# Optimization experiments

Hardware: AMD Instinct MI355X
Metric: run time of the kernel (lower is better)

Reference implementation:

```python
import jax, jax.numpy as jnp
import numpy as np

B, C, S, L = 8, 512, 2048, 8921


def setup_inputs() -> dict:
    key = jax.random.key(0)
    k1, k2, k3, k4, k5 = jax.random.split(key, 5)
    return {
        "encoded": jax.random.normal(k1, (B, C, S), dtype=jnp.float32),
        "W_attn": jax.random.normal(k2, (L, C), dtype=jnp.float32) * 0.02,
        "b_attn": jax.random.normal(k3, (L,), dtype=jnp.float32) * 0.02,
        "W_cls": jax.random.normal(k4, (L, C), dtype=jnp.float32) * 0.02,
        "b_cls": jax.random.normal(k5, (L,), dtype=jnp.float32) * 0.02,
    }


def reference(encoded, W_attn, b_attn, W_cls, b_cls):
    # encoded: (B, C, S). Linear over channels after transpose -> scores (B, S, L)
    scores = jnp.einsum("bcs,lc->bsl", encoded, W_attn) + b_attn
    # softmax over the sequence dimension (dim=1 of (B, S, L))
    weights = jax.nn.softmax(scores, axis=1)
    # context: (B, L, S) @ (B, S, C) -> (B, L, C)
    context = jnp.einsum("bsl,bcs->blc", weights, encoded)
    # per-label diagonal classifier: elementwise multiply with (L, C) weight, reduce C
    logits = jnp.sum(context * W_cls, axis=2) + b_cls  # (B, L)
    return logits
```

## Files before the change

### kernel.cpp

```cpp
#include <hip/hip_runtime.h>
#include <hip/hip_bf16.h>
#include <stdint.h>

#define B_ 8
#define C_ 512
#define S_ 2048
#define L_ 8921
#define LTILE 128
#define NLT 70
#define BS 128
#define SCHUNK 512
#define NSC 4
#define BK 64
#define ROUNDS 32

using f32x4 = __attribute__((ext_vector_type(4))) float;
using s16x8 = __attribute__((ext_vector_type(8))) short;

static __device__ __forceinline__ unsigned short f2bf(float f) {
    union { float f; uint32_t u; } a; a.f = f;
    uint32_t u = a.u;
    return (unsigned short)((u + 0x7fffu + ((u >> 16) & 1u)) >> 16);
}

__global__ void cvt_w(const float* __restrict__ src, unsigned short* __restrict__ dst, int n4) {
    int i = blockIdx.x * 256 + threadIdx.x;
    if (i >= n4) return;
    float4 v = ((const float4*)src)[i];
    ushort4 o;
    o.x = f2bf(v.x); o.y = f2bf(v.y); o.z = f2bf(v.z); o.w = f2bf(v.w);
    ((ushort4*)dst)[i] = o;
}

__global__ void cvt_e(const float* __restrict__ enc, unsigned short* __restrict__ ebt) {
    __shared__ float tile[64][65];
    int x = blockIdx.x;
    int ct = (x & 7) * 64;
    int st = ((x >> 3) & 31) * 64;
    int b  = x >> 8;
    int t = threadIdx.x;
    const float* src = enc + (size_t)b * C_ * S_;
    #pragma unroll
    for (int it = 0; it < 16; ++it) {
        int idx = it * 256 + t;
        int rc = idx >> 6, rs = idx & 63;
        tile[rc][rs] = src[(size_t)(ct + rc) * S_ + st + rs];
    }
    __syncthreads();
    unsigned short* dst = ebt + (size_t)b * S_ * C_;
    #pragma unroll
    for (int it = 0; it < 16; ++it) {
        int idx = it * 256 + t;
        int rs = idx >> 6, rc = idx & 63;
        dst[(size_t)(st + rs) * C_ + ct + rc] = f2bf(tile[rc][rs]);
    }
}

__global__ __launch_bounds__(256, 2) void attn_main(
    const unsigned short* __restrict__ ebt,
    const unsigned short* __restrict__ wa,
    const unsigned short* __restrict__ wc,
    float* __restrict__ pnum, float* __restrict__ pden)
{
    __shared__ __align__(16) unsigned char sE[32768];

    const int tid  = threadIdx.x;
    const int lane = tid & 63;
    const int wave = tid >> 6;

    const int x  = blockIdx.x;
    const int lt = x >> 5;
    const int rb = x & 31;
    const int b  = rb >> 2;
    const int sc = rb & 3;
    const int l0 = lt * LTILE;

    int rowOff[2];
    #pragma unroll
    for (int mf = 0; mf < 2; ++mf) {
        int gl = l0 + wave * 32 + mf * 16 + (lane & 15);
        if (gl > L_ - 1) gl = L_ - 1;
        rowOff[mf] = gl * C_ + ((lane >> 4) << 3);
    }

    const size_t ebase = (size_t)b * S_ * C_;
    const int kgsrcE = (((lane & 7) ^ ((lane >> 3) & 7)) << 3);
    const int rowPart = (lane & 15) << 7;
    const int laneQ = lane >> 4;
    const int laneX = lane & 7;

    struct W4 { s16x8 a0, a1, c0, c1; };
    auto loadW = [&](int rr, int k) -> W4 {
        const int co = ((rr & 7) << 6) + (k << 5);
        W4 w;
        w.a0 = *(const s16x8*)(wa + rowOff[0] + co);
        w.a1 = *(const s16x8*)(wa + rowOff[1] + co);
        w.c0 = *(const s16x8*)(wc + rowOff[0] + co);
        w.c1 = *(const s16x8*)(wc + rowOff[1] + co);
        return w;
    };

    auto stageE = [&](int rr2) {
        const int c0s = (rr2 & 7) << 6;
        const int sBase = sc * SCHUNK + (rr2 >> 3) * BS;
        unsigned char* dbase = sE + ((rr2 & 1) << 14);
        #pragma unroll
        for (int jj = 0; jj < 4; ++jj) {
            const int j = wave * 4 + jj;
            const int sg = sBase + j * 8 + (lane >> 3);
            const unsigned short* g = ebt + ebase + (size_t)sg * C_ + c0s + kgsrcE;
            __builtin_amdgcn_global_load_lds(
                (__attribute__((address_space(1))) void*)g,
                (__attribute__((address_space(3))) void*)(dbase + j * 1024),
                16, 0, 0);
        }
    };

    f32x4 accS[2][8], accV[2][8];
    #pragma unroll
    for (int mf = 0; mf < 2; ++mf)
        #pragma unroll
        for (int nf = 0; nf < 8; ++nf) {
            accS[mf][nf] = (f32x4){0.f, 0.f, 0.f, 0.f};
            accV[mf][nf] = (f32x4){0.f, 0.f, 0.f, 0.f};
        }
    float numAcc[2][4], denAcc[2][4];
    #pragma unroll
    for (int mf = 0; mf < 2; ++mf)
        #pragma unroll
        for (int r = 0; r < 4; ++r) { numAcc[mf][r] = 0.f; denAcc[mf][r] = 0.f; }

    stageE(0);
    W4 wcur = loadW(0, 0);
    asm volatile("s_waitcnt vmcnt(0)" ::: "memory");
    __builtin_amdgcn_s_barrier();
    __builtin_amdgcn_sched_barrier(0);

    for (int rr = 0; rr < ROUNDS; ++rr) {
        if (rr + 1 < ROUNDS) stageE(rr + 1);
        __builtin_amdgcn_sched_barrier(0);
        W4 wnxt = loadW(rr, 1);

        const unsigned char* fb = sE + ((rr & 1) << 14);
        {
            s16x8 fe[8];
            #pragma unroll
            for (int nf = 0; nf < 8; ++nf) {
                const int off = (nf << 11) + rowPart + ((((0 * 4) + laneQ) ^ laneX) << 4);
                fe[nf] = *(const s16x8*)(fb + off);
            }
            __builtin_amdgcn_s_setprio(1);
            #pragma unroll
            for (int nf = 0; nf < 8; ++nf) {
                accS[0][nf] = __builtin_amdgcn_mfma_f32_16x16x32_bf16(wcur.a0, fe[nf], accS[0][nf], 0, 0, 0);
                accS[1][nf] = __builtin_amdgcn_mfma_f32_16x16x32_bf16(wcur.a1, fe[nf], accS[1][nf], 0, 0, 0);
                accV[0][nf] = __builtin_amdgcn_mfma_f32_16x16x32_bf16(wcur.c0, fe[nf], accV[0][nf], 0, 0, 0);
                accV[1][nf] = __builtin_amdgcn_mfma_f32_16x16x32_bf16(wcur.c1, fe[nf], accV[1][nf], 0, 0, 0);
            }
            __builtin_amdgcn_s_setprio(0);
        }
        W4 wfut = (rr + 1 < ROUNDS) ? loadW(rr + 1, 0) : wcur;
        {
            s16x8 fe[8];
            #pragma unroll
            for (int nf = 0; nf < 8; ++nf) {
                const int off = (nf << 11) + rowPart + (((4 + laneQ) ^ laneX) << 4);
                fe[nf] = *(const s16x8*)(fb + off);
            }
            __builtin_amdgcn_s_setprio(1);
            #pragma unroll
            for (int nf = 0; nf < 8; ++nf) {
                accS[0][nf] = __builtin_amdgcn_mfma_f32_16x16x32_bf16(wnxt.a0, fe[nf], accS[0][nf], 0, 0, 0);
                accS[1][nf] = __builtin_amdgcn_mfma_f32_16x16x32_bf16(wnxt.a1, fe[nf], accS[1][nf], 0, 0, 0);
                accV[0][nf] = __builtin_amdgcn_mfma_f32_16x16x32_bf16(wnxt.c0, fe[nf], accV[0][nf], 0, 0, 0);
                accV[1][nf] = __builtin_amdgcn_mfma_f32_16x16x32_bf16(wnxt.c1, fe[nf], accV[1][nf], 0, 0, 0);
            }
            __builtin_amdgcn_s_setprio(0);
        }
        wcur = wfut;

        if ((rr & 7) == 7) {
            #pragma unroll
            for (int mf = 0; mf < 2; ++mf)
                #pragma unroll
                for (int nf = 0; nf < 8; ++nf)
                    #pragma unroll
                    for (int r = 0; r < 4; ++r) {
                        float e = __expf(accS[mf][nf][r]);
                        denAcc[mf][r] += e;
                        numAcc[mf][r] += e * accV[mf][nf][r];
                        accS[mf][nf][r] = 0.f;
                        accV[mf][nf][r] = 0.f;
                    }
        }

        __builtin_amdgcn_sched_barrier(0);
        asm volatile("s_waitcnt vmcnt(4)" ::: "memory");
        __builtin_amdgcn_s_barrier();
        __builtin_amdgcn_sched_barrier(0);
    }

    const size_t obase = ((size_t)((b * NLT + lt) * NSC + sc)) * LTILE;
    #pragma unroll
    for (int mf = 0; mf < 2; ++mf)
        #pragma unroll
        for (int r = 0; r < 4; ++r) {
            float n = numAcc[mf][r], d = denAcc[mf][r];
            n += __shfl_xor(n, 1);  d += __shfl_xor(d, 1);
            n += __shfl_xor(n, 2);  d += __shfl_xor(d, 2);
            n += __shfl_xor(n, 4);  d += __shfl_xor(d, 4);
            n += __shfl_xor(n, 8);  d += __shfl_xor(d, 8);
            if ((lane & 15) == 0) {
                int row = wave * 32 + mf * 16 + (lane >> 4) * 4 + r;
                pnum[obase + row] = n;
                pden[obase + row] = d;
            }
        }
}

__global__ void finalize(const float* __restrict__ pnum, const float* __restrict__ pden,
                         const float* __restrict__ bcls, float* __restrict__ out) {
    int gid = blockIdx.x * 256 + threadIdx.x;
    if (gid >= B_ * L_) return;
    int b = gid / L_, l = gid - b * L_;
    int lt = l >> 7, row = l & 127;
    float n = 0.f, d = 0.f;
    #pragma unroll
    for (int s = 0; s < NSC; ++s) {
        size_t idx = ((size_t)((b * NLT + lt) * NSC + s)) * LTILE + row;
        n += pnum[idx];
        d += pden[idx];
    }
    out[gid] = n / d + bcls[l];
}

extern "C" void kernel_launch(void* const* d_in, const int* in_sizes, int n_in,
                              void* d_out, int out_size, void* d_ws, size_t ws_size,
                              hipStream_t stream) {
    (void)in_sizes; (void)n_in; (void)out_size; (void)ws_size;
    const float* enc  = (const float*)d_in[0];
    const float* Wa   = (const float*)d_in[1];
    const float* Wc   = (const float*)d_in[3];
    const float* bcls = (const float*)d_in[4];

    unsigned char* ws = (unsigned char*)d_ws;
    const size_t oEbt = 0;
    const size_t oWa  = oEbt + 16777216;
    const size_t oWc  = oWa + 9136128;
    const size_t oPn  = oWc + 9136128;
    const size_t oPd  = oPn + 1146880;

    unsigned short* ebt  = (unsigned short*)(ws + oEbt);
    unsigned short* waBf = (unsigned short*)(ws + oWa);
    unsigned short* wcBf = (unsigned short*)(ws + oWc);
    float* pnum = (float*)(ws + oPn);
    float* pden = (float*)(ws + oPd);

    const int n4 = (L_ * C_) / 4;
    cvt_w<<<(n4 + 255) / 256, 256, 0, stream>>>(Wa, waBf, n4);
    cvt_w<<<(n4 + 255) / 256, 256, 0, stream>>>(Wc, wcBf, n4);
    cvt_e<<<B_ * 32 * 8, 256, 0, stream>>>(enc, ebt);
    attn_main<<<NLT * 32, 256, 0, stream>>>(ebt, waBf, wcBf, pnum, pden);
    finalize<<<(B_ * L_ + 255) / 256, 256, 0, stream>>>(pnum, pden, bcls, (float*)d_out);
}
```

Measured before the change: 432.2 us.

## Switch fused attention GEMM from 16x16x32 to 32x32x16 bf16 MFMA tiles

Replaces the 16x16x32 MFMA tiling (2x8 fragments per wave) with 32x32x16 MFMA instructions over four 32-column sequence tiles, restructuring weight loads into four k-steps per round and remapping LDS fragment addresses and output reduction rows. Larger MFMA tiles mean fewer instructions and fewer LDS fragment reads per unit of work, which raises operand reuse. The cost is more k-steps with smaller weight loads, a changed vmcnt wait, and a new output row mapping that has to be correct.

```diff
diff --git a/kernel.cpp b/kernel.cpp
--- a/kernel.cpp
+++ b/kernel.cpp
@@ -14,8 +14,9 @@
 #define BK 64
 #define ROUNDS 32
 
-using f32x4 = __attribute__((ext_vector_type(4))) float;
-using s16x8 = __attribute__((ext_vector_type(8))) short;
+using f32x4  = __attribute__((ext_vector_type(4)))  float;
+using f32x16 = __attribute__((ext_vector_type(16))) float;
+using s16x8  = __attribute__((ext_vector_type(8)))  short;
 
 static __device__ __forceinline__ unsigned short f2bf(float f) {
     union { float f; uint32_t u; } a; a.f = f;
@@ -75,28 +76,20 @@
     const int sc = rb & 3;
     const int l0 = lt * LTILE;
 
-    int rowOff[2];
-    #pragma unroll
-    for (int mf = 0; mf < 2; ++mf) {
-        int gl = l0 + wave * 32 + mf * 16 + (lane & 15);
-        if (gl > L_ - 1) gl = L_ - 1;
-        rowOff[mf] = gl * C_ + ((lane >> 4) << 3);
-    }
+    int gl = l0 + wave * 32 + (lane & 31);
+    if (gl > L_ - 1) gl = L_ - 1;
+    const int rowOffW = gl * C_ + ((lane >> 5) << 3);
 
     const size_t ebase = (size_t)b * S_ * C_;
     const int kgsrcE = (((lane & 7) ^ ((lane >> 3) & 7)) << 3);
-    const int rowPart = (lane & 15) << 7;
-    const int laneQ = lane >> 4;
-    const int laneX = lane & 7;
-
-    struct W4 { s16x8 a0, a1, c0, c1; };
-    auto loadW = [&](int rr, int k) -> W4 {
-        const int co = ((rr & 7) << 6) + (k << 5);
-        W4 w;
-        w.a0 = *(const s16x8*)(wa + rowOff[0] + co);
-        w.a1 = *(const s16x8*)(wa + rowOff[1] + co);
-        w.c0 = *(const s16x8*)(wc + rowOff[0] + co);
-        w.c1 = *(const s16x8*)(wc + rowOff[1] + co);
+    const int feBase = ((lane & 31) << 7) + ((((lane >> 5) ^ (lane & 7))) << 4);
+
+    struct W2 { s16x8 a, c; };
+    auto loadW = [&](int rr, int k) -> W2 {
+        const int co = ((rr & 7) << 6) + (k << 4);
+        W2 w;
+        w.a = *(const s16x8*)(wa + rowOffW + co);
+        w.c = *(const s16x8*)(wc + rowOffW + co);
         return w;
     };
 
@@ -116,22 +109,17 @@
         }
     };
 
-    f32x4 accS[2][8], accV[2][8];
-    #pragma unroll
-    for (int mf = 0; mf < 2; ++mf)
+    f32x16 accS[4], accV[4];
+    #pragma unroll
+    for (int t = 0; t < 4; ++t)
         #pragma unroll
-        for (int nf = 0; nf < 8; ++nf) {
-            accS[mf][nf] = (f32x4){0.f, 0.f, 0.f, 0.f};
-            accV[mf][nf] = (f32x4){0.f, 0.f, 0.f, 0.f};
-        }
-    float numAcc[2][4], denAcc[2][4];
-    #pragma unroll
-    for (int mf = 0; mf < 2; ++mf)
-        #pragma unroll
-        for (int r = 0; r < 4; ++r) { numAcc[mf][r] = 0.f; denAcc[mf][r] = 0.f; }
+        for (int r = 0; r < 16; ++r) { accS[t][r] = 0.f; accV[t][r] = 0.f; }
+    float numAcc[16], denAcc[16];
+    #pragma unroll
+    for (int r = 0; r < 16; ++r) { numAcc[r] = 0.f; denAcc[r] = 0.f; }
 
     stageE(0);
-    W4 wcur = loadW(0, 0);
+    W2 wk = loadW(0, 0);
     asm volatile("s_waitcnt vmcnt(0)" ::: "memory");
     __builtin_amdgcn_s_barrier();
     __builtin_amdgcn_sched_barrier(0);
@@ -139,83 +127,66 @@
     for (int rr = 0; rr < ROUNDS; ++rr) {
         if (rr + 1 < ROUNDS) stageE(rr + 1);
         __builtin_amdgcn_sched_barrier(0);
-        W4 wnxt = loadW(rr, 1);
 
         const unsigned char* fb = sE + ((rr & 1) << 14);
-        {
-            s16x8 fe[8];
+
+        #pragma unroll
+        for (int kstep = 0; kstep < 4; ++kstep) {
+            W2 wn;
+            if (kstep < 3)              wn = loadW(rr, kstep + 1);
+            else if (rr + 1 < ROUNDS)   wn = loadW(rr + 1, 0);
+            else                        wn = wk;
+
+            s16x8 fe[4];
+            const int addrK = feBase ^ (kstep << 5);
             #pragma unroll
-            for (int nf = 0; nf < 8; ++nf) {
-                const int off = (nf << 11) + rowPart + ((((0 * 4) + laneQ) ^ laneX) << 4);
-                fe[nf] = *(const s16x8*)(fb + off);
-            }
+            for (int t = 0; t < 4; ++t)
+                fe[t] = *(const s16x8*)(fb + (t << 12) + addrK);
+
             __builtin_amdgcn_s_setprio(1);
             #pragma unroll
-            for (int nf = 0; nf < 8; ++nf) {
-                accS[0][nf] = __builtin_amdgcn_mfma_f32_16x16x32_bf16(wcur.a0, fe[nf], accS[0][nf], 0, 0, 0);
-                accS[1][nf] = __builtin_amdgcn_mfma_f32_16x16x32_bf16(wcur.a1, fe[nf], accS[1][nf], 0, 0, 0);
-                accV[0][nf] = __builtin_amdgcn_mfma_f32_16x16x32_bf16(wcur.c0, fe[nf], accV[0][nf], 0, 0, 0);
-                accV[1][nf] = __builtin_amdgcn_mfma_f32_16x16x32_bf16(wcur.c1, fe[nf], accV[1][nf], 0, 0, 0);
+            for (int t = 0; t < 4; ++t) {
+                accS[t] = __builtin_amdgcn_mfma_f32_32x32x16_bf16(wk.a, fe[t], accS[t], 0, 0, 0);
+                accV[t] = __builtin_amdgcn_mfma_f32_32x32x16_bf16(wk.c, fe[t], accV[t], 0, 0, 0);
             }
             __builtin_amdgcn_s_setprio(0);
-        }
-        W4 wfut = (rr + 1 < ROUNDS) ? loadW(rr + 1, 0) : wcur;
-        {
-            s16x8 fe[8];
-            #pragma unroll
-            for (int nf = 0; nf < 8; ++nf) {
-                const int off = (nf << 11) + rowPart + (((4 + laneQ) ^ laneX) << 4);
-                fe[nf] = *(const s16x8*)(fb + off);
-            }
-            __builtin_amdgcn_s_setprio(1);
-            #pragma unroll
-            for (int nf = 0; nf < 8; ++nf) {
-                accS[0][nf] = __builtin_amdgcn_mfma_f32_16x16x32_bf16(wnxt.a0, fe[nf], accS[0][nf], 0, 0, 0);
-                accS[1][nf] = __builtin_amdgcn_mfma_f32_16x16x32_bf16(wnxt.a1, fe[nf], accS[1][nf], 0, 0, 0);
-                accV[0][nf] = __builtin_amdgcn_mfma_f32_16x16x32_bf16(wnxt.c0, fe[nf], accV[0][nf], 0, 0, 0);
-                accV[1][nf] = __builtin_amdgcn_mfma_f32_16x16x32_bf16(wnxt.c1, fe[nf], accV[1][nf], 0, 0, 0);
-            }
-            __builtin_amdgcn_s_setprio(0);
-        }
-        wcur = wfut;
+            wk = wn;
+        }
 
         if ((rr & 7) == 7) {
             #pragma unroll
-            for (int mf = 0; mf < 2; ++mf)
+            for (int t = 0; t < 4; ++t)
                 #pragma unroll
-                for (int nf = 0; nf < 8; ++nf)
-                    #pragma unroll
-                    for (int r = 0; r < 4; ++r) {
-                        float e = __expf(accS[mf][nf][r]);
-                        denAcc[mf][r] += e;
-                        numAcc[mf][r] += e * accV[mf][nf][r];
-                        accS[mf][nf][r] = 0.f;
-                        accV[mf][nf][r] = 0.f;
-                    }
+                for (int r = 0; r < 16; ++r) {
+                    float e = __expf(accS[t][r]);
+                    denAcc[r] += e;
+                    numAcc[r] += e * accV[t][r];
+                    accS[t][r] = 0.f;
+                    accV[t][r] = 0.f;
+                }
         }
 
         __builtin_amdgcn_sched_barrier(0);
-        asm volatile("s_waitcnt vmcnt(4)" ::: "memory");
+        asm volatile("s_waitcnt vmcnt(2)" ::: "memory");
         __builtin_amdgcn_s_barrier();
         __builtin_amdgcn_sched_barrier(0);
     }
 
     const size_t obase = ((size_t)((b * NLT + lt) * NSC + sc)) * LTILE;
     #pragma unroll
-    for (int mf = 0; mf < 2; ++mf)
-        #pragma unroll
-        for (int r = 0; r < 4; ++r) {
-            float n = numAcc[mf][r], d = denAcc[mf][r];
-            n += __shfl_xor(n, 1);  d += __shfl_xor(d, 1);
-            n += __shfl_xor(n, 2);  d += __shfl_xor(d, 2);
-            n += __shfl_xor(n, 4);  d += __shfl_xor(d, 4);
-            n += __shfl_xor(n, 8);  d += __shfl_xor(d, 8);
-            if ((lane & 15) == 0) {
-                int row = wave * 32 + mf * 16 + (lane >> 4) * 4 + r;
-                pnum[obase + row] = n;
-                pden[obase + row] = d;
-            }
-        }
+    for (int r = 0; r < 16; ++r) {
+        float n = numAcc[r], d = denAcc[r];
+        n += __shfl_xor(n, 1);   d += __shfl_xor(d, 1);
+        n += __shfl_xor(n, 2);   d += __shfl_xor(d, 2);
+        n += __shfl_xor(n, 4);   d += __shfl_xor(d, 4);
+        n += __shfl_xor(n, 8);   d += __shfl_xor(d, 8);
+        n += __shfl_xor(n, 16);  d += __shfl_xor(d, 16);
+        if ((lane & 31) == 0) {
+            int row = wave * 32 + (r & 3) + ((r >> 2) << 3) + ((lane >> 5) << 2);
+            pnum[obase + row] = n;
+            pden[obase + row] = d;
+        }
+    }
 }
 
 __global__ void finalize(const float* __restrict__ pnum, const float* __restrict__ pden,
```

New measurement: 456.9 us. 5.7% more time.

## Split block into 2x2 wave grid with per-wave private LDS staging, no barriers

Applied to the files above, without the earlier changes.

Changes the wave decomposition from four waves each covering 32 labels across all 128 sequence positions to a 2x2 grid: 64 labels by 256 sequence positions per wave. Each wave stages its own encoded slice into a private double-buffered LDS region, so the per-round block-wide barrier goes away and only vmcnt waits remain. Weight fragments are loaded inside the round rather than prefetched a round ahead. Partial num/den sums from the two sequence-half waves are combined in LDS at the end. The cost is that weight loads are no longer prefetched across rounds and each wave issues more global loads into LDS.

```diff
diff --git a/kernel.cpp b/kernel.cpp
--- a/kernel.cpp
+++ b/kernel.cpp
@@ -8,7 +8,6 @@
 #define L_ 8921
 #define LTILE 128
 #define NLT 70
-#define BS 128
 #define SCHUNK 512
 #define NSC 4
 #define BK 64
@@ -62,128 +61,130 @@
     const unsigned short* __restrict__ wc,
     float* __restrict__ pnum, float* __restrict__ pden)
 {
-    __shared__ __align__(16) unsigned char sE[32768];
+    __shared__ __align__(16) unsigned char sE[4][16384];
+    __shared__ float red[2][2][128];
 
     const int tid  = threadIdx.x;
     const int lane = tid & 63;
     const int wave = tid >> 6;
+    const int wL   = wave & 1;
+    const int wS   = wave >> 1;
 
     const int x  = blockIdx.x;
     const int lt = x >> 5;
     const int rb = x & 31;
     const int b  = rb >> 2;
     const int sc = rb & 3;
-    const int l0 = lt * LTILE;
-
-    int rowOff[2];
-    #pragma unroll
-    for (int mf = 0; mf < 2; ++mf) {
-        int gl = l0 + wave * 32 + mf * 16 + (lane & 15);
+
+    int rowOffW[4];
+    #pragma unroll
+    for (int mf = 0; mf < 4; ++mf) {
+        int gl = lt * LTILE + wL * 64 + mf * 16 + (lane & 15);
         if (gl > L_ - 1) gl = L_ - 1;
-        rowOff[mf] = gl * C_ + ((lane >> 4) << 3);
+        rowOffW[mf] = gl * C_ + ((lane >> 4) << 3);
     }
 
     const size_t ebase = (size_t)b * S_ * C_;
+    const int sWave = sc * SCHUNK + wS * 256;
     const int kgsrcE = (((lane & 7) ^ ((lane >> 3) & 7)) << 3);
-    const int rowPart = (lane & 15) << 7;
+    const int feRow = (lane & 15) << 7;
     const int laneQ = lane >> 4;
     const int laneX = lane & 7;
 
-    struct W4 { s16x8 a0, a1, c0, c1; };
-    auto loadW = [&](int rr, int k) -> W4 {
-        const int co = ((rr & 7) << 6) + (k << 5);
-        W4 w;
-        w.a0 = *(const s16x8*)(wa + rowOff[0] + co);
-        w.a1 = *(const s16x8*)(wa + rowOff[1] + co);
-        w.c0 = *(const s16x8*)(wc + rowOff[0] + co);
-        w.c1 = *(const s16x8*)(wc + rowOff[1] + co);
-        return w;
-    };
+    unsigned char* myb = sE[wave];
 
     auto stageE = [&](int rr2) {
-        const int c0s = (rr2 & 7) << 6;
-        const int sBase = sc * SCHUNK + (rr2 >> 3) * BS;
-        unsigned char* dbase = sE + ((rr2 & 1) << 14);
-        #pragma unroll
-        for (int jj = 0; jj < 4; ++jj) {
-            const int j = wave * 4 + jj;
-            const int sg = sBase + j * 8 + (lane >> 3);
-            const unsigned short* g = ebt + ebase + (size_t)sg * C_ + c0s + kgsrcE;
+        const int kcolS = (rr2 & 7) << 6;
+        const int sBase = sWave + ((rr2 >> 3) << 6);
+        unsigned char* dbase = myb + ((rr2 & 1) << 13);
+        #pragma unroll
+        for (int jj = 0; jj < 8; ++jj) {
+            const int sg = sBase + jj * 8 + (lane >> 3);
+            const unsigned short* g = ebt + ebase + (size_t)sg * C_ + kcolS + kgsrcE;
             __builtin_amdgcn_global_load_lds(
                 (__attribute__((address_space(1))) void*)g,
-                (__attribute__((address_space(3))) void*)(dbase + j * 1024),
+                (__attribute__((address_space(3))) void*)(dbase + jj * 1024),
                 16, 0, 0);
         }
     };
 
-    f32x4 accS[2][8], accV[2][8];
-    #pragma unroll
-    for (int mf = 0; mf < 2; ++mf)
-        #pragma unroll
-        for (int nf = 0; nf < 8; ++nf) {
+    f32x4 accS[4][4], accV[4][4];
+    #pragma unroll
+    for (int mf = 0; mf < 4; ++mf)
+        #pragma unroll
+        for (int nf = 0; nf < 4; ++nf) {
             accS[mf][nf] = (f32x4){0.f, 0.f, 0.f, 0.f};
             accV[mf][nf] = (f32x4){0.f, 0.f, 0.f, 0.f};
         }
-    float numAcc[2][4], denAcc[2][4];
-    #pragma unroll
-    for (int mf = 0; mf < 2; ++mf)
+    float numAcc[4][4], denAcc[4][4];
+    #pragma unroll
+    for (int mf = 0; mf < 4; ++mf)
         #pragma unroll
         for (int r = 0; r < 4; ++r) { numAcc[mf][r] = 0.f; denAcc[mf][r] = 0.f; }
 
     stageE(0);
-    W4 wcur = loadW(0, 0);
-    asm volatile("s_waitcnt vmcnt(0)" ::: "memory");
-    __builtin_amdgcn_s_barrier();
-    __builtin_amdgcn_sched_barrier(0);
 
     for (int rr = 0; rr < ROUNDS; ++rr) {
-        if (rr + 1 < ROUNDS) stageE(rr + 1);
+        const int kcol = (rr & 7) << 6;
+
+        s16x8 wA0[4], wC0[4], wA1[4], wC1[4];
+        #pragma unroll
+        for (int mf = 0; mf < 4; ++mf) {
+            wA0[mf] = *(const s16x8*)(wa + rowOffW[mf] + kcol);
+            wC0[mf] = *(const s16x8*)(wc + rowOffW[mf] + kcol);
+        }
+        #pragma unroll
+        for (int mf = 0; mf < 4; ++mf) {
+            wA1[mf] = *(const s16x8*)(wa + rowOffW[mf] + kcol + 32);
+            wC1[mf] = *(const s16x8*)(wc + rowOffW[mf] + kcol + 32);
+        }
+        if (rr + 1 < ROUNDS) {
+            stageE(rr + 1);
+            __builtin_amdgcn_sched_barrier(0);
+            asm volatile("s_waitcnt vmcnt(24)" ::: "memory");
+        } else {
+            __builtin_amdgcn_sched_barrier(0);
+            asm volatile("s_waitcnt vmcnt(16)" ::: "memory");
+        }
         __builtin_amdgcn_sched_barrier(0);
-        W4 wnxt = loadW(rr, 1);
-
-        const unsigned char* fb = sE + ((rr & 1) << 14);
+
+        const unsigned char* fb = myb + ((rr & 1) << 13);
         {
-            s16x8 fe[8];
-            #pragma unroll
-            for (int nf = 0; nf < 8; ++nf) {
-                const int off = (nf << 11) + rowPart + ((((0 * 4) + laneQ) ^ laneX) << 4);
-                fe[nf] = *(const s16x8*)(fb + off);
-            }
+            s16x8 fe[4];
+            #pragma unroll
+            for (int nf = 0; nf < 4; ++nf)
+                fe[nf] = *(const s16x8*)(fb + (nf << 11) + feRow + (((laneQ) ^ laneX) << 4));
             __builtin_amdgcn_s_setprio(1);
             #pragma unroll
-            for (int nf = 0; nf < 8; ++nf) {
-                accS[0][nf] = __builtin_amdgcn_mfma_f32_16x16x32_bf16(wcur.a0, fe[nf], accS[0][nf], 0, 0, 0);
-                accS[1][nf] = __builtin_amdgcn_mfma_f32_16x16x32_bf16(wcur.a1, fe[nf], accS[1][nf], 0, 0, 0);
-                accV[0][nf] = __builtin_amdgcn_mfma_f32_16x16x32_bf16(wcur.c0, fe[nf], accV[0][nf], 0, 0, 0);
-                accV[1][nf] = __builtin_amdgcn_mfma_f32_16x16x32_bf16(wcur.c1, fe[nf], accV[1][nf], 0, 0, 0);
-            }
+            for (int nf = 0; nf < 4; ++nf)
+                #pragma unroll
+                for (int mf = 0; mf < 4; ++mf) {
+                    accS[mf][nf] = __builtin_amdgcn_mfma_f32_16x16x32_bf16(wA0[mf], fe[nf], accS[mf][nf], 0, 0, 0);
+                    accV[mf][nf] = __builtin_amdgcn_mfma_f32_16x16x32_bf16(wC0[mf], fe[nf], accV[mf][nf], 0, 0, 0);
+                }
             __builtin_amdgcn_s_setprio(0);
         }
-        W4 wfut = (rr + 1 < ROUNDS) ? loadW(rr + 1, 0) : wcur;
         {
-            s16x8 fe[8];
-            #pragma unroll
-            for (int nf = 0; nf < 8; ++nf) {
-                const int off = (nf << 11) + rowPart + (((4 + laneQ) ^ laneX) << 4);
-                fe[nf] = *(const s16x8*)(fb + off);
-            }
+            s16x8 fe[4];
+            #pragma unroll
+            for (int nf = 0; nf < 4; ++nf)
+                fe[nf] = *(const s16x8*)(fb + (nf << 11) + feRow + (((4 + laneQ) ^ laneX) << 4));
             __builtin_amdgcn_s_setprio(1);
             #pragma unroll
-            for (int nf = 0; nf < 8; ++nf) {
-                accS[0][nf] = __builtin_amdgcn_mfma_f32_16x16x32_bf16(wnxt.a0, fe[nf], accS[0][nf], 0, 0, 0);
-                accS[1][nf] = __builtin_amdgcn_mfma_f32_16x16x32_bf16(wnxt.a1, fe[nf], accS[1][nf], 0, 0, 0);
-                accV[0][nf] = __builtin_amdgcn_mfma_f32_16x16x32_bf16(wnxt.c0, fe[nf], accV[0][nf], 0, 0, 0);
-                accV[1][nf] = __builtin_amdgcn_mfma_f32_16x16x32_bf16(wnxt.c1, fe[nf], accV[1][nf], 0, 0, 0);
-            }
+            for (int nf = 0; nf < 4; ++nf)
+                #pragma unroll
+                for (int mf = 0; mf < 4; ++mf) {
+                    accS[mf][nf] = __builtin_amdgcn_mfma_f32_16x16x32_bf16(wA1[mf], fe[nf], accS[mf][nf], 0, 0, 0);
+                    accV[mf][nf] = __builtin_amdgcn_mfma_f32_16x16x32_bf16(wC1[mf], fe[nf], accV[mf][nf], 0, 0, 0);
+                }
             __builtin_amdgcn_s_setprio(0);
         }
-        wcur = wfut;
 
         if ((rr & 7) == 7) {
             #pragma unroll
-            for (int mf = 0; mf < 2; ++mf)
+            for (int mf = 0; mf < 4; ++mf)
                 #pragma unroll
-                for (int nf = 0; nf < 8; ++nf)
+                for (int nf = 0; nf < 4; ++nf)
                     #pragma unroll
                     for (int r = 0; r < 4; ++r) {
                         float e = __expf(accS[mf][nf][r]);
@@ -193,16 +194,10 @@
                         accV[mf][nf][r] = 0.f;
                     }
         }
-
-        __builtin_amdgcn_sched_barrier(0);
-        asm volatile("s_waitcnt vmcnt(4)" ::: "memory");
-        __builtin_amdgcn_s_barrier();
-        __builtin_amdgcn_sched_barrier(0);
-    }
-
-    const size_t obase = ((size_t)((b * NLT + lt) * NSC + sc)) * LTILE;
-    #pragma unroll
-    for (int mf = 0; mf < 2; ++mf)
+    }
+
+    #pragma unroll
+    for (int mf = 0; mf < 4; ++mf)
         #pragma unroll
         for (int r = 0; r < 4; ++r) {
             float n = numAcc[mf][r], d = denAcc[mf][r];
@@ -211,11 +206,19 @@
             n += __shfl_xor(n, 4);  d += __shfl_xor(d, 4);
             n += __shfl_xor(n, 8);  d += __shfl_xor(d, 8);
             if ((lane & 15) == 0) {
-                int row = wave * 32 + mf * 16 + (lane >> 4) * 4 + r;
-                pnum[obase + row] = n;
-                pden[obase + row] = d;
+                int row = wL * 64 + mf * 16 + (lane >> 4) * 4 + r;
+                red[wS][0][row] = n;
+                red[wS][1][row] = d;
             }
         }
+    __syncthreads();
+    {
+        const size_t obase = ((size_t)((b * NLT + lt) * NSC + sc)) * LTILE;
+        int row = tid & 127, nd = tid >> 7;
+        float v = red[0][nd][row] + red[1][nd][row];
+        float* dst = nd ? pden : pnum;
+        dst[obase + row] = v;
+    }
 }
 
 __global__ void finalize(const float* __restrict__ pnum, const float* __restrict__ pden,
```

Result: slower. 738.6 us (+70.9%).

## Double K-tile depth per round to halve barrier count, stagger block starts

Applied to the files above, without the earlier changes.

Each round now stages a 128-channel K slice of the encoded tile into a 64KB double-buffered LDS region instead of 64 channels, halving the rounds and the barriers per sequence chunk. The inner loop runs four K sub-steps with rolling weight prefetch, and the swizzle is reworked for 256-byte rows. It also adds an s_sleep to every other group of 256 blocks to stagger memory traffic at launch. The larger LDS footprint per block may drop occupancy below the declared two blocks per CU, and the sleep adds a small delay to half the blocks.

```diff
diff --git a/kernel.cpp b/kernel.cpp
--- a/kernel.cpp
+++ b/kernel.cpp
@@ -11,8 +11,8 @@
 #define BS 128
 #define SCHUNK 512
 #define NSC 4
-#define BK 64
-#define ROUNDS 32
+#define BK 128
+#define ROUNDS 16
 
 using f32x4 = __attribute__((ext_vector_type(4))) float;
 using s16x8 = __attribute__((ext_vector_type(8))) short;
@@ -62,7 +62,7 @@
     const unsigned short* __restrict__ wc,
     float* __restrict__ pnum, float* __restrict__ pden)
 {
-    __shared__ __align__(16) unsigned char sE[32768];
+    __shared__ __align__(16) unsigned char sE[65536];
 
     const int tid  = threadIdx.x;
     const int lane = tid & 63;
@@ -75,6 +75,8 @@
     const int sc = rb & 3;
     const int l0 = lt * LTILE;
 
+    if ((x >> 8) & 1) asm volatile("s_sleep 48");
+
     int rowOff[2];
     #pragma unroll
     for (int mf = 0; mf < 2; ++mf) {
@@ -84,14 +86,13 @@
     }
 
     const size_t ebase = (size_t)b * S_ * C_;
-    const int kgsrcE = (((lane & 7) ^ ((lane >> 3) & 7)) << 3);
-    const int rowPart = (lane & 15) << 7;
     const int laneQ = lane >> 4;
     const int laneX = lane & 7;
+    const int feRow = (lane & 15) << 8;
 
     struct W4 { s16x8 a0, a1, c0, c1; };
-    auto loadW = [&](int rr, int k) -> W4 {
-        const int co = ((rr & 7) << 6) + (k << 5);
+    auto loadW = [&](int rr, int ks) -> W4 {
+        const int co = ((rr & 3) << 7) + (ks << 5);
         W4 w;
         w.a0 = *(const s16x8*)(wa + rowOff[0] + co);
         w.a1 = *(const s16x8*)(wa + rowOff[1] + co);
@@ -101,14 +102,15 @@
     };
 
     auto stageE = [&](int rr2) {
-        const int c0s = (rr2 & 7) << 6;
-        const int sBase = sc * SCHUNK + (rr2 >> 3) * BS;
-        unsigned char* dbase = sE + ((rr2 & 1) << 14);
-        #pragma unroll
-        for (int jj = 0; jj < 4; ++jj) {
-            const int j = wave * 4 + jj;
-            const int sg = sBase + j * 8 + (lane >> 3);
-            const unsigned short* g = ebt + ebase + (size_t)sg * C_ + c0s + kgsrcE;
+        const int c0s = (rr2 & 3) << 7;
+        const int sBase = sc * SCHUNK + ((rr2 >> 2) << 7);
+        unsigned char* dbase = sE + ((rr2 & 1) << 15);
+        #pragma unroll
+        for (int jj = 0; jj < 8; ++jj) {
+            const int j = wave * 8 + jj;
+            const int sg = sBase + j * 4 + (lane >> 4);
+            const int srcChunk = (lane & 15) ^ (((j & 1) << 2) + (lane >> 4));
+            const unsigned short* g = ebt + ebase + (size_t)sg * C_ + c0s + (srcChunk << 3);
             __builtin_amdgcn_global_load_lds(
                 (__attribute__((address_space(1))) void*)g,
                 (__attribute__((address_space(3))) void*)(dbase + j * 1024),
@@ -139,16 +141,22 @@
     for (int rr = 0; rr < ROUNDS; ++rr) {
         if (rr + 1 < ROUNDS) stageE(rr + 1);
         __builtin_amdgcn_sched_barrier(0);
-        W4 wnxt = loadW(rr, 1);
-
-        const unsigned char* fb = sE + ((rr & 1) << 14);
-        {
+
+        const unsigned char* fb = sE + ((rr & 1) << 15);
+
+        #pragma unroll
+        for (int ks = 0; ks < 4; ++ks) {
+            W4 wnxt;
+            if (ks < 3)                wnxt = loadW(rr, ks + 1);
+            else if (rr + 1 < ROUNDS)  wnxt = loadW(rr + 1, 0);
+            else                       wnxt = wcur;
+
             s16x8 fe[8];
+            const int chunkX = (((ks << 2) + laneQ) ^ laneX) << 4;
             #pragma unroll
-            for (int nf = 0; nf < 8; ++nf) {
-                const int off = (nf << 11) + rowPart + ((((0 * 4) + laneQ) ^ laneX) << 4);
-                fe[nf] = *(const s16x8*)(fb + off);
-            }
+            for (int nf = 0; nf < 8; ++nf)
+                fe[nf] = *(const s16x8*)(fb + (nf << 12) + feRow + chunkX);
+
             __builtin_amdgcn_s_setprio(1);
             #pragma unroll
             for (int nf = 0; nf < 8; ++nf) {
@@ -158,28 +166,10 @@
                 accV[1][nf] = __builtin_amdgcn_mfma_f32_16x16x32_bf16(wcur.c1, fe[nf], accV[1][nf], 0, 0, 0);
             }
             __builtin_amdgcn_s_setprio(0);
-        }
-        W4 wfut = (rr + 1 < ROUNDS) ? loadW(rr + 1, 0) : wcur;
-        {
-            s16x8 fe[8];
-            #pragma unroll
-            for (int nf = 0; nf < 8; ++nf) {
-                const int off = (nf << 11) + rowPart + (((4 + laneQ) ^ laneX) << 4);
-                fe[nf] = *(const s16x8*)(fb + off);
-            }
-            __builtin_amdgcn_s_setprio(1);
-            #pragma unroll
-            for (int nf = 0; nf < 8; ++nf) {
-                accS[0][nf] = __builtin_amdgcn_mfma_f32_16x16x32_bf16(wnxt.a0, fe[nf], accS[0][nf], 0, 0, 0);
-                accS[1][nf] = __builtin_amdgcn_mfma_f32_16x16x32_bf16(wnxt.a1, fe[nf], accS[1][nf], 0, 0, 0);
-                accV[0][nf] = __builtin_amdgcn_mfma_f32_16x16x32_bf16(wnxt.c0, fe[nf], accV[0][nf], 0, 0, 0);
-                accV[1][nf] = __builtin_amdgcn_mfma_f32_16x16x32_bf16(wnxt.c1, fe[nf], accV[1][nf], 0, 0, 0);
-            }
-            __builtin_amdgcn_s_setprio(0);
-        }
-        wcur = wfut;
-
-        if ((rr & 7) == 7) {
+            wcur = wnxt;
+        }
+
+        if ((rr & 3) == 3) {
             #pragma unroll
             for (int mf = 0; mf < 2; ++mf)
                 #pragma unroll
```

New measurement: 415.8 us. -3.8%, faster.
